# Optimization experiments

Hardware: AMD Instinct MI355X
Metric: run time of the kernel (lower is better)

Reference implementation:

```python
import jax, jax.numpy as jnp
import numpy as np

NUM_HEADS = 16

def setup_inputs() -> dict:
    key = jax.random.key(0)
    ks = jax.random.split(key, 9)
    E = 1024
    T, B = 2048, 2
    s = E ** -0.5
    return {
        "query": jax.random.normal(ks[0], (T, B, E), dtype=jnp.float32),
        "Wq": jax.random.normal(ks[1], (E, E), dtype=jnp.float32) * s,
        "bq": jax.random.normal(ks[2], (E,), dtype=jnp.float32) * 0.02,
        "Wk": jax.random.normal(ks[3], (E, E), dtype=jnp.float32) * s,
        "bk": jax.random.normal(ks[4], (E,), dtype=jnp.float32) * 0.02,
        "Wv": jax.random.normal(ks[5], (E, E), dtype=jnp.float32) * s,
        "bv": jax.random.normal(ks[6], (E,), dtype=jnp.float32) * 0.02,
        "Wo": jax.random.normal(ks[7], (E, E), dtype=jnp.float32) * s,
        "bo": jax.random.normal(ks[8], (E,), dtype=jnp.float32) * 0.02,
    }

def reference(query, Wq, bq, Wk, bk, Wv, bv, Wo, bo):
    # query: [T, B, E] (seq-first, fairseq/ESM layout)
    T, B, E = query.shape
    H = NUM_HEADS
    D = E // H
    scaling = D ** -0.5
    # projections (eqx Linear: x @ W.T + b); note k/v also come from `query` (self-attention)
    q = (query @ Wq.T + bq) * scaling
    k = query @ Wk.T + bk
    v = query @ Wv.T + bv
    # [T, B, E] -> [B*H, T, D]
    q = q.reshape(T, B * H, D).transpose(1, 0, 2)
    k = k.reshape(T, B * H, D).transpose(1, 0, 2)
    v = v.reshape(T, B * H, D).transpose(1, 0, 2)
    # full score matrix [B*H, T, T], softmax in fp32 (as in original)
    scores = jnp.einsum('ntd,nsd->nts', q, k)
    attn_w = jax.nn.softmax(scores.astype(jnp.float32), axis=-1)
    attn = jnp.einsum('nts,nsd->ntd', attn_w.astype(v.dtype), v)
    # [B*H, T, D] -> [T, B, E]
    attn = attn.transpose(1, 0, 2).reshape(T, B, E)
    return attn @ Wo.T + bo
```

## Files before the change

### kernel.cpp

```cpp
#include <hip/hip_runtime.h>
#include <hip/hip_bf16.h>


typedef __attribute__((ext_vector_type(8))) short short8;
typedef __attribute__((ext_vector_type(4))) float f32x4;
typedef __attribute__((ext_vector_type(16))) float f32x16;
typedef __attribute__((ext_vector_type(4))) unsigned u32x4;

#define T_DIM 2048
#define B_DIM 2
#define E_DIM 1024
#define H_DIM 16
#define D_DIM 64
#define M_ROWS (T_DIM * B_DIM)
#define QKV_N (3 * E_DIM)
#define HEAD_ELEMS (32 * 2048 * 64)
#define LOG2E 1.44269504088896340736f

__device__ __forceinline__ unsigned short f2bf(float f) {
    unsigned u = __builtin_bit_cast(unsigned, f);
    unsigned r = (u + 0x7fffu + ((u >> 16) & 1u)) >> 16;
    return (unsigned short)r;
}

__device__ __forceinline__ unsigned cvt_pk_bf16(float lo, float hi) {
    unsigned d;
    asm("v_cvt_pk_bf16_f32 %0, %1, %2" : "=v"(d) : "v"(lo), "v"(hi));
    return d;
}

__device__ __forceinline__ void gload_lds16(const void* g, void* l) {
    __builtin_amdgcn_global_load_lds(
        (const __attribute__((address_space(1))) void*)g,
        (__attribute__((address_space(3))) void*)l, 16, 0, 0);
}

__device__ __forceinline__ f32x16 mfma32(short8 a, short8 b, f32x16 c) {
    return __builtin_amdgcn_mfma_f32_32x32x16_bf16(a, b, c, 0, 0, 0);
}

__global__ __launch_bounds__(256) void cast_all(
    const float* __restrict__ X,
    const float* __restrict__ Wq, const float* __restrict__ Wk,
    const float* __restrict__ Wv, const float* __restrict__ Wo,
    unsigned short* __restrict__ Xbf,
    unsigned short* __restrict__ Wcat,
    unsigned short* __restrict__ Wobf)
{
    int idx = blockIdx.x * 256 + threadIdx.x;
    size_t base = (size_t)idx * 8;
    int row = (int)(base >> 10);
    int col = (int)(base & 1023);
    const float* src;
    unsigned short* dst;
    float scale = 1.0f;
    if (row < 4096) {
        src = X + base;
        dst = Xbf + base;
    } else if (row < 7168) {
        int wrow = row - 4096;
        if (wrow < 1024)      { src = Wq + ((size_t)wrow << 10) + col; scale = 0.125f * LOG2E; }
        else if (wrow < 2048) { src = Wk + ((size_t)(wrow - 1024) << 10) + col; }
        else                  { src = Wv + ((size_t)(wrow - 2048) << 10) + col; }
        dst = Wcat + ((size_t)wrow << 10) + col;
    } else {
        int wrow = row - 7168;
        src = Wo + ((size_t)wrow << 10) + col;
        dst = Wobf + ((size_t)wrow << 10) + col;
    }
    float4 f0 = *(const float4*)src;
    float4 f1 = *(const float4*)(src + 4);
    short8 r;
    r[0] = (short)f2bf(f0.x * scale);
    r[1] = (short)f2bf(f0.y * scale);
    r[2] = (short)f2bf(f0.z * scale);
    r[3] = (short)f2bf(f0.w * scale);
    r[4] = (short)f2bf(f1.x * scale);
    r[5] = (short)f2bf(f1.y * scale);
    r[6] = (short)f2bf(f1.z * scale);
    r[7] = (short)f2bf(f1.w * scale);
    *(short8*)dst = r;
}

__global__ __launch_bounds__(256) void bias_fuse(
    const float* __restrict__ bq, const float* __restrict__ bk,
    const float* __restrict__ bv, float* __restrict__ biasq)
{
    int i = blockIdx.x * 256 + threadIdx.x;
    if (i < 1024)       biasq[i] = 0.125f * LOG2E * bq[i];
    else if (i < 2048)  biasq[i] = bk[i - 1024];
    else if (i < 3072)  biasq[i] = bv[i - 2048];
}

template <int MODE>
__global__ __launch_bounds__(256) void gemm_bt(
    const unsigned short* __restrict__ A,
    const unsigned short* __restrict__ B,
    const float* __restrict__ bias,
    void* __restrict__ outp,
    int M, int N, int K)
{
    __shared__ alignas(16) unsigned short As[3][128 * 32];
    __shared__ alignas(16) unsigned short Bs[3][128 * 32];
    const int tid = threadIdx.x;
    const int wave = tid >> 6, lane = tid & 63;
    const int lr = lane & 15, lg = lane >> 4;
    const int nbx = N >> 7;
    const int bx = blockIdx.x % nbx, by = blockIdx.x / nbx;
    const int wr = wave >> 1, wc = wave & 1;

    f32x4 acc[4][4] = {};

    auto stage = [&](int slot, int kt) {
#pragma unroll
        for (int pass = 0; pass < 2; ++pass) {
            int c = pass * 256 + wave * 64 + lane;
            int row = c >> 2, kc = c & 3;
            gload_lds16(A + (size_t)(by * 128 + row) * K + kt + kc * 8,
                        (char*)&As[slot][0] + c * 16);
            gload_lds16(B + (size_t)(bx * 128 + row) * K + kt + kc * 8,
                        (char*)&Bs[slot][0] + c * 16);
        }
    };

    const int NK = K >> 5;
    stage(0, 0);
    stage(1, 32);
    int s3 = 0;
    for (int ki = 0; ki < NK; ++ki) {
        asm volatile("s_waitcnt lgkmcnt(0)" ::: "memory");
        if (ki < NK - 1) asm volatile("s_waitcnt vmcnt(4)" ::: "memory");
        else             asm volatile("s_waitcnt vmcnt(0)" ::: "memory");
        __builtin_amdgcn_s_barrier();
        __builtin_amdgcn_sched_barrier(0);
        if (ki + 2 < NK) {
            int ns = s3 + 2; if (ns >= 3) ns -= 3;
            stage(ns, (ki + 2) * 32);
        }

        short8 af[4], bf[4];
#pragma unroll
        for (int m = 0; m < 4; ++m)
            af[m] = *(const short8*)&As[s3][(wr * 64 + m * 16 + lr) * 32 + lg * 8];
#pragma unroll
        for (int n = 0; n < 4; ++n)
            bf[n] = *(const short8*)&Bs[s3][(wc * 64 + n * 16 + lr) * 32 + lg * 8];
        __builtin_amdgcn_s_setprio(1);
#pragma unroll
        for (int m = 0; m < 4; ++m)
#pragma unroll
            for (int n = 0; n < 4; ++n)
                acc[m][n] = __builtin_amdgcn_mfma_f32_16x16x32_bf16(af[m], bf[n], acc[m][n], 0, 0, 0);
        __builtin_amdgcn_s_setprio(0);

        s3 = (s3 + 1 == 3) ? 0 : s3 + 1;
    }

    const int gcol0 = bx * 128 + wc * 64;
    const int grow0 = by * 128 + wr * 64;
    if (MODE == 0) {
        unsigned short* qb = (unsigned short*)outp;
#pragma unroll
        for (int m = 0; m < 4; ++m) {
#pragma unroll
            for (int n = 0; n < 4; ++n) {
                int col = gcol0 + n * 16 + lr;
                float bsv = bias[col];
                int which = col >> 10;
                int e = col & 1023;
                int h = e >> 6, d = e & 63;
                if (which < 2) {
                    unsigned short* bufb = qb + (size_t)which * HEAD_ELEMS;
#pragma unroll
                    for (int j = 0; j < 4; ++j) {
                        int r = grow0 + m * 16 + lg * 4 + j;
                        int t = r >> 1, b = r & 1;
                        int bh = b * 16 + h;
                        bufb[((size_t)bh * 2048 + t) * 64 + d] = f2bf(acc[m][n][j] + bsv);
                    }
                } else {
                    unsigned* vT32 = (unsigned*)(qb + (size_t)2 * HEAD_ELEMS);
                    int t0 = (grow0 + m * 16 + lg * 4) >> 1;
                    int dwidx = t0 >> 1;
                    int dwp = (dwidx & ~6) | ((dwidx & 2) << 1) | ((dwidx & 4) >> 1);
                    unsigned w0 = (unsigned)f2bf(acc[m][n][0] + bsv) |
                                  ((unsigned)f2bf(acc[m][n][2] + bsv) << 16);
                    unsigned w1 = (unsigned)f2bf(acc[m][n][1] + bsv) |
                                  ((unsigned)f2bf(acc[m][n][3] + bsv) << 16);
                    vT32[(size_t)(h * 64 + d) * 1024 + dwp] = w0;
                    vT32[(size_t)((16 + h) * 64 + d) * 1024 + dwp] = w1;
                }
            }
        }
    } else {
        float* O = (float*)outp;
#pragma unroll
        for (int m = 0; m < 4; ++m) {
#pragma unroll
            for (int n = 0; n < 4; ++n) {
                int col = gcol0 + n * 16 + lr;
                float bsv = bias[col];
#pragma unroll
                for (int j = 0; j < 4; ++j) {
                    int r = grow0 + m * 16 + lg * 4 + j;
                    O[(size_t)r * N + col] = acc[m][n][j] + bsv;
                }
            }
        }
    }
}

struct AttnCtx {
    const unsigned short* kh;
    const unsigned short* vh;
    int tid, ql, hi;
};

template<bool DO_PV, bool DO_STAGE, bool LASTWAIT>
__device__ __forceinline__ void attn_step(
    const AttnCtx& cx, int kt_next,
    const char* Kb, const char* Vprv, char* Kst, char* Vst,
    const short8 (&qv)[4],
    const short8 (&paP)[4], short8 (&paC)[4],
    f32x16 (&accO)[2], float& lrun)
{
    const int tid = cx.tid, ql = cx.ql, hi = cx.hi;
    asm volatile("s_waitcnt lgkmcnt(0)" ::: "memory");
    if constexpr (LASTWAIT) asm volatile("s_waitcnt vmcnt(0)" ::: "memory");
    else                    asm volatile("s_waitcnt vmcnt(4)" ::: "memory");
    __builtin_amdgcn_s_barrier();
    __builtin_amdgcn_sched_barrier(0);

    if constexpr (DO_STAGE) {
#pragma unroll
        for (int p = 0; p < 2; ++p) {
            int c = p * 256 + tid;
            int row = c >> 3;
            int sxb = ((c & 7) * 16) ^ ((row & 7) << 4);
            gload_lds16(cx.kh + (size_t)(kt_next + row) * 64 + (sxb >> 1), Kst + c * 16);
        }
#pragma unroll
        for (int p = 0; p < 2; ++p) {
            int c = p * 256 + tid;
            int d = c >> 3;
            int sxb = ((c & 7) * 16) ^ ((d & 7) << 4);
            gload_lds16(cx.vh + (size_t)d * 2048 + kt_next + (sxb >> 1), Vst + c * 16);
        }
    }

    f32x16 st[2] = {};
    __builtin_amdgcn_s_setprio(1);
#pragma unroll
    for (int m = 0; m < 2; ++m) {
        int krow = m * 32 + ql;
#pragma unroll
        for (int c = 0; c < 4; ++c) {
            int bo = (krow * 128 + c * 32 + hi * 16) ^ ((krow & 7) << 4);
            short8 ka = *(const short8*)(Kb + bo);
            st[m] = mfma32(ka, qv[c], st[m]);
        }
    }
    if constexpr (DO_PV) {
#pragma unroll
        for (int n = 0; n < 2; ++n) {
            int d = n * 32 + ql;
#pragma unroll
            for (int kc = 0; kc < 4; ++kc) {
                int bo = (d * 128 + kc * 32 + hi * 16) ^ ((d & 7) << 4);
                short8 va = *(const short8*)(Vprv + bo);
                accO[n] = mfma32(va, paP[kc], accO[n]);
            }
        }
    }
    __builtin_amdgcn_s_setprio(0);
    __builtin_amdgcn_sched_barrier(0);

    float rs0 = 0.f, rs1 = 0.f, rs2 = 0.f, rs3 = 0.f;
#pragma unroll
    for (int m = 0; m < 2; ++m) {
#pragma unroll
        for (int r = 0; r < 16; r += 4) {
            float e0 = __builtin_amdgcn_exp2f(st[m][r + 0]);
            float e1 = __builtin_amdgcn_exp2f(st[m][r + 1]);
            float e2 = __builtin_amdgcn_exp2f(st[m][r + 2]);
            float e3 = __builtin_amdgcn_exp2f(st[m][r + 3]);
            st[m][r + 0] = e0; st[m][r + 1] = e1;
            st[m][r + 2] = e2; st[m][r + 3] = e3;
            rs0 += e0; rs1 += e1; rs2 += e2; rs3 += e3;
        }
    }
    lrun += (rs0 + rs1) + (rs2 + rs3);

#pragma unroll
    for (int kc = 0; kc < 4; ++kc) {
        int m = kc >> 1, b8 = (kc & 1) * 8;
        u32x4 u;
        u[0] = cvt_pk_bf16(st[m][b8 + 0], st[m][b8 + 1]);
        u[1] = cvt_pk_bf16(st[m][b8 + 2], st[m][b8 + 3]);
        u[2] = cvt_pk_bf16(st[m][b8 + 4], st[m][b8 + 5]);
        u[3] = cvt_pk_bf16(st[m][b8 + 6], st[m][b8 + 7]);
        paC[kc] = __builtin_bit_cast(short8, u);
    }
}

__global__ __launch_bounds__(256, 2) void attn_fwd(
    const unsigned short* __restrict__ q,
    const unsigned short* __restrict__ k,
    const unsigned short* __restrict__ vT,
    unsigned short* __restrict__ outb)
{
    __shared__ alignas(16) unsigned short Ks[3][64 * 64];
    __shared__ alignas(16) unsigned short Vs[4][64 * 64];
    const int tid = threadIdx.x, wv = tid >> 6, l = tid & 63;
    const int ql = l & 31, hi = l >> 5;
    const int lid = blockIdx.x;
    const int xcd = lid & 7, slot = lid >> 3;
    const int bh = xcd * 4 + (slot >> 4);
    const int q0 = (slot & 15) * 128;
    const unsigned short* qh = q + (size_t)bh * (2048 * 64);
    AttnCtx cx;
    cx.kh = k + (size_t)bh * (2048 * 64);
    cx.vh = vT + (size_t)bh * (64 * 2048);
    cx.tid = tid; cx.ql = ql; cx.hi = hi;

#define KSLOT(i) ((char*)&Ks[i][0])
#define VSLOT(i) ((char*)&Vs[i][0])

    const int qrow = q0 + wv * 32 + ql;
    short8 qv[4];
#pragma unroll
    for (int c = 0; c < 4; ++c)
        qv[c] = *(const short8*)&qh[(size_t)qrow * 64 + c * 16 + hi * 8];

    f32x16 accO[2] = {};
    float lrun = 0.0f;
    short8 paA[4], paB[4];

#pragma unroll
    for (int tt = 0; tt < 2; ++tt) {
#pragma unroll
        for (int p = 0; p < 2; ++p) {
            int c = p * 256 + tid;
            int row = c >> 3;
            int sxb = ((c & 7) * 16) ^ ((row & 7) << 4);
            gload_lds16(cx.kh + (size_t)(tt * 64 + row) * 64 + (sxb >> 1),
                        KSLOT(tt) + c * 16);
        }
#pragma unroll
        for (int p = 0; p < 2; ++p) {
            int c = p * 256 + tid;
            int d = c >> 3;
            int sxb = ((c & 7) * 16) ^ ((d & 7) << 4);
            gload_lds16(cx.vh + (size_t)d * 2048 + tt * 64 + (sxb >> 1),
                        VSLOT(tt) + c * 16);
        }
    }

    int k3 = 0, v4 = 0;
    auto adv = [&]() { k3 = (k3 + 1 == 3) ? 0 : k3 + 1; v4 = (v4 + 1) & 3; };

    attn_step<false, true, false>(cx, 2 * 64, KSLOT(0), nullptr,
                                  KSLOT(2), VSLOT(2),
                                  qv, paB, paA, accO, lrun);
    adv();
    for (int t = 1; t <= 27; t += 2) {
        int ns3 = (k3 + 2 >= 3) ? k3 - 1 : k3 + 2;
        attn_step<true, true, false>(cx, (t + 2) * 64,
                                     KSLOT(k3), VSLOT((v4 + 3) & 3),
                                     KSLOT(ns3), VSLOT((v4 + 2) & 3),
                                     qv, paA, paB, accO, lrun);
        adv();
        ns3 = (k3 + 2 >= 3) ? k3 - 1 : k3 + 2;
        attn_step<true, true, false>(cx, (t + 3) * 64,
                                     KSLOT(k3), VSLOT((v4 + 3) & 3),
                                     KSLOT(ns3), VSLOT((v4 + 2) & 3),
                                     qv, paB, paA, accO, lrun);
        adv();
    }
    {
        int ns3 = (k3 + 2 >= 3) ? k3 - 1 : k3 + 2;
        attn_step<true, true, false>(cx, 31 * 64,
                                     KSLOT(k3), VSLOT((v4 + 3) & 3),
                                     KSLOT(ns3), VSLOT((v4 + 2) & 3),
                                     qv, paA, paB, accO, lrun);
        adv();
    }
    attn_step<true, false, false>(cx, 0, KSLOT(k3), VSLOT((v4 + 3) & 3),
                                  nullptr, nullptr,
                                  qv, paB, paA, accO, lrun);
    adv();
    attn_step<true, false, true>(cx, 0, KSLOT(k3), VSLOT((v4 + 3) & 3),
                                 nullptr, nullptr,
                                 qv, paA, paB, accO, lrun);
#pragma unroll
    for (int n = 0; n < 2; ++n) {
        int d = n * 32 + ql;
#pragma unroll
        for (int kc = 0; kc < 4; ++kc) {
            int bo = (d * 128 + kc * 32 + hi * 16) ^ ((d & 7) << 4);
            short8 va = *(const short8*)(VSLOT(3) + bo);
            accO[n] = mfma32(va, paB[kc], accO[n]);
        }
    }

    const float ltot = lrun + __shfl_xor(lrun, 32);
    const float inv = 1.0f / ltot;
    const int b = bh >> 4, h = bh & 15;
    const int orow = qrow * 2 + b;
#pragma unroll
    for (int n = 0; n < 2; ++n)
#pragma unroll
        for (int rq = 0; rq < 4; ++rq) {
            uint2 u;
            u.x = cvt_pk_bf16(accO[n][rq * 4 + 0] * inv, accO[n][rq * 4 + 1] * inv);
            u.y = cvt_pk_bf16(accO[n][rq * 4 + 2] * inv, accO[n][rq * 4 + 3] * inv);
            *(uint2*)&outb[(size_t)orow * 1024 + h * 64 + n * 32 + rq * 8 + hi * 4] = u;
        }
#undef KSLOT
#undef VSLOT
}

extern "C" void kernel_launch(void* const* d_in, const int* in_sizes, int n_in,
                              void* d_out, int out_size, void* d_ws, size_t ws_size,
                              hipStream_t stream) {
    const float* X  = (const float*)d_in[0];
    const float* Wq = (const float*)d_in[1];
    const float* bq = (const float*)d_in[2];
    const float* Wk = (const float*)d_in[3];
    const float* bk = (const float*)d_in[4];
    const float* Wv = (const float*)d_in[5];
    const float* bv = (const float*)d_in[6];
    const float* Wo = (const float*)d_in[7];
    const float* bo = (const float*)d_in[8];
    float* out = (float*)d_out;

    char* ws = (char*)d_ws;
    if (ws_size < ((size_t)49 << 20)) return;
    unsigned short* Xbf   = (unsigned short*)(ws);
    unsigned short* Wcat  = (unsigned short*)(ws + ((size_t)8  << 20));
    unsigned short* Wobf  = (unsigned short*)(ws + ((size_t)14 << 20));
    unsigned short* qb    = (unsigned short*)(ws + ((size_t)16 << 20));
    unsigned short* ab    = (unsigned short*)(ws + ((size_t)40 << 20));
    float*          biasq = (float*)(ws + ((size_t)48 << 20));
    unsigned short* kb  = qb + (size_t)HEAD_ELEMS;
    unsigned short* vTb = qb + (size_t)2 * HEAD_ELEMS;

    cast_all<<<4096, 256, 0, stream>>>(X, Wq, Wk, Wv, Wo, Xbf, Wcat, Wobf);
    bias_fuse<<<12, 256, 0, stream>>>(bq, bk, bv, biasq);
    gemm_bt<0><<<dim3((M_ROWS / 128) * (QKV_N / 128)), 256, 0, stream>>>(
        Xbf, Wcat, biasq, (void*)qb, M_ROWS, QKV_N, E_DIM);
    attn_fwd<<<dim3(32 * 16), 256, 0, stream>>>(qb, kb, vTb, ab);
    gemm_bt<1><<<dim3((M_ROWS / 128) * (E_DIM / 128)), 256, 0, stream>>>(
        ab, Wobf, bo, (void*)out, M_ROWS, E_DIM, E_DIM);
}
```

Measured before the change: 119.4 us.

## Unroll ring-buffer pipelines with static LDS slots and fold bias kernel into cast

The GEMM and attention main loops are unrolled by the ring-buffer period (3 stages for GEMM, 4 K/V slots for attention) so every LDS slot pointer is a compile-time constant, removing the modular slot arithmetic. The explicit lgkmcnt(0) wait before each barrier is dropped. The separate bias_fuse launch is merged into cast_all as one extra block, saving a kernel launch. The GEMM loop now hardcodes K=1024, and dropping the LDS wait relies on the compiler inserting correct waits before the reads.

New measurement: 115.8 us. 1.03x faster.

```diff
diff --git a/kernel.cpp b/kernel.cpp
--- a/kernel.cpp
+++ b/kernel.cpp
@@ -43,11 +43,25 @@
     const float* __restrict__ X,
     const float* __restrict__ Wq, const float* __restrict__ Wk,
     const float* __restrict__ Wv, const float* __restrict__ Wo,
+    const float* __restrict__ bq, const float* __restrict__ bk,
+    const float* __restrict__ bv,
     unsigned short* __restrict__ Xbf,
     unsigned short* __restrict__ Wcat,
-    unsigned short* __restrict__ Wobf)
+    unsigned short* __restrict__ Wobf,
+    float* __restrict__ biasq)
 {
     int idx = blockIdx.x * 256 + threadIdx.x;
+    if (idx >= (1 << 20)) {
+        int i = idx - (1 << 20);
+        for (int j = i; j < 3072; j += 256) {
+            float v;
+            if (j < 1024)       v = 0.125f * LOG2E * bq[j];
+            else if (j < 2048)  v = bk[j - 1024];
+            else                v = bv[j - 2048];
+            biasq[j] = v;
+        }
+        return;
+    }
     size_t base = (size_t)idx * 8;
     int row = (int)(base >> 10);
     int col = (int)(base & 1023);
@@ -82,14 +96,53 @@
     *(short8*)dst = r;
 }
 
-__global__ __launch_bounds__(256) void bias_fuse(
-    const float* __restrict__ bq, const float* __restrict__ bk,
-    const float* __restrict__ bv, float* __restrict__ biasq)
-{
-    int i = blockIdx.x * 256 + threadIdx.x;
-    if (i < 1024)       biasq[i] = 0.125f * LOG2E * bq[i];
-    else if (i < 2048)  biasq[i] = bk[i - 1024];
-    else if (i < 3072)  biasq[i] = bv[i - 2048];
+struct GemmCtx {
+    const unsigned short* A;
+    const unsigned short* B;
+    int K, by, bx, wave, lane, wr, wc, lr, lg;
+};
+
+__device__ __forceinline__ void gemm_stage(
+    const GemmCtx& g, unsigned short* Ast, unsigned short* Bst, int kt)
+{
+#pragma unroll
+    for (int pass = 0; pass < 2; ++pass) {
+        int c = pass * 256 + g.wave * 64 + g.lane;
+        int row = c >> 2, kc = c & 3;
+        gload_lds16(g.A + (size_t)(g.by * 128 + row) * g.K + kt + kc * 8,
+                    (char*)Ast + c * 16);
+        gload_lds16(g.B + (size_t)(g.bx * 128 + row) * g.K + kt + kc * 8,
+                    (char*)Bst + c * 16);
+    }
+}
+
+template <bool DO_STAGE, bool LASTWAIT>
+__device__ __forceinline__ void gemm_step(
+    const GemmCtx& g,
+    unsigned short* Acs, unsigned short* Bcs,
+    unsigned short* Ast, unsigned short* Bst, int kt_next,
+    f32x4 (&acc)[4][4])
+{
+    if constexpr (LASTWAIT) asm volatile("s_waitcnt vmcnt(0)" ::: "memory");
+    else                    asm volatile("s_waitcnt vmcnt(4)" ::: "memory");
+    __builtin_amdgcn_s_barrier();
+    __builtin_amdgcn_sched_barrier(0);
+    if constexpr (DO_STAGE) gemm_stage(g, Ast, Bst, kt_next);
+
+    short8 af[4], bf[4];
+#pragma unroll
+    for (int m = 0; m < 4; ++m)
+        af[m] = *(const short8*)&Acs[(g.wr * 64 + m * 16 + g.lr) * 32 + g.lg * 8];
+#pragma unroll
+    for (int n = 0; n < 4; ++n)
+        bf[n] = *(const short8*)&Bcs[(g.wc * 64 + n * 16 + g.lr) * 32 + g.lg * 8];
+    __builtin_amdgcn_s_setprio(1);
+#pragma unroll
+    for (int m = 0; m < 4; ++m)
+#pragma unroll
+        for (int n = 0; n < 4; ++n)
+            acc[m][n] = __builtin_amdgcn_mfma_f32_16x16x32_bf16(af[m], bf[n], acc[m][n], 0, 0, 0);
+    __builtin_amdgcn_s_setprio(0);
 }
 
 template <int MODE>
@@ -109,52 +162,23 @@
     const int bx = blockIdx.x % nbx, by = blockIdx.x / nbx;
     const int wr = wave >> 1, wc = wave & 1;
 
+    GemmCtx g{A, B, K, by, bx, wave, lane, wr, wc, lr, lg};
     f32x4 acc[4][4] = {};
 
-    auto stage = [&](int slot, int kt) {
-#pragma unroll
-        for (int pass = 0; pass < 2; ++pass) {
-            int c = pass * 256 + wave * 64 + lane;
-            int row = c >> 2, kc = c & 3;
-            gload_lds16(A + (size_t)(by * 128 + row) * K + kt + kc * 8,
-                        (char*)&As[slot][0] + c * 16);
-            gload_lds16(B + (size_t)(bx * 128 + row) * K + kt + kc * 8,
-                        (char*)&Bs[slot][0] + c * 16);
-        }
-    };
-
-    const int NK = K >> 5;
-    stage(0, 0);
-    stage(1, 32);
-    int s3 = 0;
-    for (int ki = 0; ki < NK; ++ki) {
-        asm volatile("s_waitcnt lgkmcnt(0)" ::: "memory");
-        if (ki < NK - 1) asm volatile("s_waitcnt vmcnt(4)" ::: "memory");
-        else             asm volatile("s_waitcnt vmcnt(0)" ::: "memory");
-        __builtin_amdgcn_s_barrier();
-        __builtin_amdgcn_sched_barrier(0);
-        if (ki + 2 < NK) {
-            int ns = s3 + 2; if (ns >= 3) ns -= 3;
-            stage(ns, (ki + 2) * 32);
-        }
-
-        short8 af[4], bf[4];
-#pragma unroll
-        for (int m = 0; m < 4; ++m)
-            af[m] = *(const short8*)&As[s3][(wr * 64 + m * 16 + lr) * 32 + lg * 8];
-#pragma unroll
-        for (int n = 0; n < 4; ++n)
-            bf[n] = *(const short8*)&Bs[s3][(wc * 64 + n * 16 + lr) * 32 + lg * 8];
-        __builtin_amdgcn_s_setprio(1);
-#pragma unroll
-        for (int m = 0; m < 4; ++m)
-#pragma unroll
-            for (int n = 0; n < 4; ++n)
-                acc[m][n] = __builtin_amdgcn_mfma_f32_16x16x32_bf16(af[m], bf[n], acc[m][n], 0, 0, 0);
-        __builtin_amdgcn_s_setprio(0);
-
-        s3 = (s3 + 1 == 3) ? 0 : s3 + 1;
-    }
+    unsigned short *A0 = &As[0][0], *A1 = &As[1][0], *A2 = &As[2][0];
+    unsigned short *B0 = &Bs[0][0], *B1 = &Bs[1][0], *B2 = &Bs[2][0];
+
+    gemm_stage(g, A0, B0, 0);
+    gemm_stage(g, A1, B1, 32);
+#pragma unroll 1
+    for (int it = 0; it < 10; ++it) {
+        int kb = it * 96;
+        gemm_step<true, false>(g, A0, B0, A2, B2, kb + 64, acc);
+        gemm_step<true, false>(g, A1, B1, A0, B0, kb + 96, acc);
+        gemm_step<true, false>(g, A2, B2, A1, B1, kb + 128, acc);
+    }
+    gemm_step<false, false>(g, A0, B0, nullptr, nullptr, 0, acc);
+    gemm_step<false, true >(g, A1, B1, nullptr, nullptr, 0, acc);
 
     const int gcol0 = bx * 128 + wc * 64;
     const int grow0 = by * 128 + wr * 64;
@@ -216,6 +240,25 @@
     int tid, ql, hi;
 };
 
+__device__ __forceinline__ void attn_stage(
+    const AttnCtx& cx, char* Kst, char* Vst, int kt)
+{
+#pragma unroll
+    for (int p = 0; p < 2; ++p) {
+        int c = p * 256 + cx.tid;
+        int row = c >> 3;
+        int sxb = ((c & 7) * 16) ^ ((row & 7) << 4);
+        gload_lds16(cx.kh + (size_t)(kt + row) * 64 + (sxb >> 1), Kst + c * 16);
+    }
+#pragma unroll
+    for (int p = 0; p < 2; ++p) {
+        int c = p * 256 + cx.tid;
+        int d = c >> 3;
+        int sxb = ((c & 7) * 16) ^ ((d & 7) << 4);
+        gload_lds16(cx.vh + (size_t)d * 2048 + kt + (sxb >> 1), Vst + c * 16);
+    }
+}
+
 template<bool DO_PV, bool DO_STAGE, bool LASTWAIT>
 __device__ __forceinline__ void attn_step(
     const AttnCtx& cx, int kt_next,
@@ -224,29 +267,13 @@
     const short8 (&paP)[4], short8 (&paC)[4],
     f32x16 (&accO)[2], float& lrun)
 {
-    const int tid = cx.tid, ql = cx.ql, hi = cx.hi;
-    asm volatile("s_waitcnt lgkmcnt(0)" ::: "memory");
+    const int ql = cx.ql, hi = cx.hi;
     if constexpr (LASTWAIT) asm volatile("s_waitcnt vmcnt(0)" ::: "memory");
     else                    asm volatile("s_waitcnt vmcnt(4)" ::: "memory");
     __builtin_amdgcn_s_barrier();
     __builtin_amdgcn_sched_barrier(0);
 
-    if constexpr (DO_STAGE) {
-#pragma unroll
-        for (int p = 0; p < 2; ++p) {
-            int c = p * 256 + tid;
-            int row = c >> 3;
-            int sxb = ((c & 7) * 16) ^ ((row & 7) << 4);
-            gload_lds16(cx.kh + (size_t)(kt_next + row) * 64 + (sxb >> 1), Kst + c * 16);
-        }
-#pragma unroll
-        for (int p = 0; p < 2; ++p) {
-            int c = p * 256 + tid;
-            int d = c >> 3;
-            int sxb = ((c & 7) * 16) ^ ((d & 7) << 4);
-            gload_lds16(cx.vh + (size_t)d * 2048 + kt_next + (sxb >> 1), Vst + c * 16);
-        }
-    }
+    if constexpr (DO_STAGE) attn_stage(cx, Kst, Vst, kt_next);
 
     f32x16 st[2] = {};
     __builtin_amdgcn_s_setprio(1);
@@ -309,7 +336,7 @@
     const unsigned short* __restrict__ vT,
     unsigned short* __restrict__ outb)
 {
-    __shared__ alignas(16) unsigned short Ks[3][64 * 64];
+    __shared__ alignas(16) unsigned short Ks[4][64 * 64];
     __shared__ alignas(16) unsigned short Vs[4][64 * 64];
     const int tid = threadIdx.x, wv = tid >> 6, l = tid & 63;
     const int ql = l & 31, hi = l >> 5;
@@ -323,8 +350,10 @@
     cx.vh = vT + (size_t)bh * (64 * 2048);
     cx.tid = tid; cx.ql = ql; cx.hi = hi;
 
-#define KSLOT(i) ((char*)&Ks[i][0])
-#define VSLOT(i) ((char*)&Vs[i][0])
+    char* K0 = (char*)&Ks[0][0]; char* K1 = (char*)&Ks[1][0];
+    char* K2 = (char*)&Ks[2][0]; char* K3 = (char*)&Ks[3][0];
+    char* V0 = (char*)&Vs[0][0]; char* V1 = (char*)&Vs[1][0];
+    char* V2 = (char*)&Vs[2][0]; char* V3 = (char*)&Vs[3][0];
 
     const int qrow = q0 + wv * 32 + ql;
     short8 qv[4];
@@ -336,61 +365,28 @@
     float lrun = 0.0f;
     short8 paA[4], paB[4];
 
-#pragma unroll
-    for (int tt = 0; tt < 2; ++tt) {
-#pragma unroll
-        for (int p = 0; p < 2; ++p) {
-            int c = p * 256 + tid;
-            int row = c >> 3;
-            int sxb = ((c & 7) * 16) ^ ((row & 7) << 4);
-            gload_lds16(cx.kh + (size_t)(tt * 64 + row) * 64 + (sxb >> 1),
-                        KSLOT(tt) + c * 16);
-        }
-#pragma unroll
-        for (int p = 0; p < 2; ++p) {
-            int c = p * 256 + tid;
-            int d = c >> 3;
-            int sxb = ((c & 7) * 16) ^ ((d & 7) << 4);
-            gload_lds16(cx.vh + (size_t)d * 2048 + tt * 64 + (sxb >> 1),
-                        VSLOT(tt) + c * 16);
-        }
-    }
-
-    int k3 = 0, v4 = 0;
-    auto adv = [&]() { k3 = (k3 + 1 == 3) ? 0 : k3 + 1; v4 = (v4 + 1) & 3; };
-
-    attn_step<false, true, false>(cx, 2 * 64, KSLOT(0), nullptr,
-                                  KSLOT(2), VSLOT(2),
+    attn_stage(cx, K0, V0, 0);
+    attn_stage(cx, K1, V1, 64);
+
+    attn_step<false, true, false>(cx, 2 * 64, K0, nullptr, K2, V2,
                                   qv, paB, paA, accO, lrun);
-    adv();
-    for (int t = 1; t <= 27; t += 2) {
-        int ns3 = (k3 + 2 >= 3) ? k3 - 1 : k3 + 2;
-        attn_step<true, true, false>(cx, (t + 2) * 64,
-                                     KSLOT(k3), VSLOT((v4 + 3) & 3),
-                                     KSLOT(ns3), VSLOT((v4 + 2) & 3),
+    attn_step<true, true, false>(cx, 3 * 64, K1, V0, K3, V3,
+                                 qv, paA, paB, accO, lrun);
+#pragma unroll 1
+    for (int it = 0; it < 7; ++it) {
+        const int t = 2 + it * 4;
+        attn_step<true, true, false>(cx, (t + 2) * 64, K2, V1, K0, V0,
+                                     qv, paB, paA, accO, lrun);
+        attn_step<true, true, false>(cx, (t + 3) * 64, K3, V2, K1, V1,
                                      qv, paA, paB, accO, lrun);
-        adv();
-        ns3 = (k3 + 2 >= 3) ? k3 - 1 : k3 + 2;
-        attn_step<true, true, false>(cx, (t + 3) * 64,
-                                     KSLOT(k3), VSLOT((v4 + 3) & 3),
-                                     KSLOT(ns3), VSLOT((v4 + 2) & 3),
+        attn_step<true, true, false>(cx, (t + 4) * 64, K0, V3, K2, V2,
                                      qv, paB, paA, accO, lrun);
-        adv();
-    }
-    {
-        int ns3 = (k3 + 2 >= 3) ? k3 - 1 : k3 + 2;
-        attn_step<true, true, false>(cx, 31 * 64,
-                                     KSLOT(k3), VSLOT((v4 + 3) & 3),
-                                     KSLOT(ns3), VSLOT((v4 + 2) & 3),
+        attn_step<true, true, false>(cx, (t + 5) * 64, K1, V0, K3, V3,
                                      qv, paA, paB, accO, lrun);
-        adv();
-    }
-    attn_step<true, false, false>(cx, 0, KSLOT(k3), VSLOT((v4 + 3) & 3),
-                                  nullptr, nullptr,
+    }
+    attn_step<true, false, false>(cx, 0, K2, V1, nullptr, nullptr,
                                   qv, paB, paA, accO, lrun);
-    adv();
-    attn_step<true, false, true>(cx, 0, KSLOT(k3), VSLOT((v4 + 3) & 3),
-                                 nullptr, nullptr,
+    attn_step<true, false, true>(cx, 0, K3, V2, nullptr, nullptr,
                                  qv, paA, paB, accO, lrun);
 #pragma unroll
     for (int n = 0; n < 2; ++n) {
@@ -398,7 +394,7 @@
 #pragma unroll
         for (int kc = 0; kc < 4; ++kc) {
             int bo = (d * 128 + kc * 32 + hi * 16) ^ ((d & 7) << 4);
-            short8 va = *(const short8*)(VSLOT(3) + bo);
+            short8 va = *(const short8*)(V3 + bo);
             accO[n] = mfma32(va, paB[kc], accO[n]);
         }
     }
@@ -416,8 +412,6 @@
             u.y = cvt_pk_bf16(accO[n][rq * 4 + 2] * inv, accO[n][rq * 4 + 3] * inv);
             *(uint2*)&outb[(size_t)orow * 1024 + h * 64 + n * 32 + rq * 8 + hi * 4] = u;
         }
-#undef KSLOT
-#undef VSLOT
 }
 
 extern "C" void kernel_launch(void* const* d_in, const int* in_sizes, int n_in,
@@ -445,8 +439,8 @@
     unsigned short* kb  = qb + (size_t)HEAD_ELEMS;
     unsigned short* vTb = qb + (size_t)2 * HEAD_ELEMS;
 
-    cast_all<<<4096, 256, 0, stream>>>(X, Wq, Wk, Wv, Wo, Xbf, Wcat, Wobf);
-    bias_fuse<<<12, 256, 0, stream>>>(bq, bk, bv, biasq);
+    cast_all<<<4097, 256, 0, stream>>>(X, Wq, Wk, Wv, Wo, bq, bk, bv,
+                                       Xbf, Wcat, Wobf, biasq);
     gemm_bt<0><<<dim3((M_ROWS / 128) * (QKV_N / 128)), 256, 0, stream>>>(
         Xbf, Wcat, biasq, (void*)qb, M_ROWS, QKV_N, E_DIM);
     attn_fwd<<<dim3(32 * 16), 256, 0, stream>>>(qb, kb, vTb, ab);
```
